# Optimization experiments

Hardware: AMD Instinct MI355X
Metric: run time of the kernel (lower is better)

## Reference

```python
import jax, jax.numpy as jnp
import numpy as np
from jax import lax

EPS = 1e-5
B, T, IN, H, D = 16, 512, 128, 256, 8


def setup_inputs() -> dict:
    key = jax.random.key(0)
    ks = jax.random.split(key, 9)
    s = 0.05  # small init to keep tanh unsaturated
    f32 = jnp.float32
    return {
        "y": jax.random.normal(ks[0], (B, T, IN), f32),
        "W_ih": jax.random.normal(ks[1], (H, IN), f32) * s,
        "W_hh": jax.random.normal(ks[2], (H, H), f32) * s,
        "b_ih": jax.random.normal(ks[3], (H,), f32) * s,
        "b_hh": jax.random.normal(ks[4], (H,), f32) * s,
        "W_mean": jax.random.normal(ks[5], (D, H), f32) * s,
        "b_mean": jax.random.normal(ks[6], (D,), f32) * s,
        "W_bd": jax.random.normal(ks[7], (2 * D, H), f32) * s,
        "b_bd": jax.random.normal(ks[8], (2 * D,), f32) * s,
    }


def _forward(y, W_ih, W_hh, b_ih, b_hh, W_mean, b_mean, W_bd, b_bd):
    # --- single-layer unidirectional tanh RNN (torch nn.RNN, batch_first) ---
    x_proj = jnp.einsum("bti,hi->bth", y, W_ih) + b_ih  # [B,T,H]

    def step(h, xt):
        h_new = jnp.tanh(xt + h @ W_hh.T + b_hh)
        return h_new, h_new

    h0 = jnp.zeros((y.shape[0], W_hh.shape[0]), y.dtype)
    _, hs = lax.scan(step, h0, jnp.swapaxes(x_proj, 0, 1))  # [T,B,H]
    enc = jnp.swapaxes(hs, 0, 1)  # [B,T,H]

    mean = enc @ W_mean.T + b_mean  # [B,T,D]
    bd = enc @ W_bd.T + b_bd        # [B,T,2D]

    d = mean.shape[-1]
    t = bd.shape[1]
    diag_e = bd[:, :, :d]        # [B,T,D]  main-diag factor elems
    off_e = bd[:, :-1, d:]       # [B,T-1,D] super-diag factor elems

    a2 = diag_e ** 2
    b2 = jnp.concatenate([jnp.zeros_like(off_e[:, :1]), off_e ** 2], axis=1)  # [B,T,D]
    ab = diag_e[:, :-1] * off_e  # [B,T-1,D]

    main = jnp.swapaxes(a2 + b2, 1, 2) + EPS  # [B,D,T]  (eps*I folded into diag)
    supd = jnp.swapaxes(ab, 1, 2)             # [B,D,T-1]

    i = jnp.arange(t)
    j = jnp.arange(t - 1)
    prec = jnp.zeros((bd.shape[0], d, t, t), bd.dtype)  # [B,D,T,T]
    prec = prec.at[:, :, i, i].set(main)
    prec = prec.at[:, :, j, j + 1].set(supd)
    prec = prec.at[:, :, j + 1, j].set(supd)
    return mean, prec


def reference(y, W_ih, W_hh, b_ih, b_hh, W_mean, b_mean, W_bd, b_bd):
    # Returns the parameters of the D per-dim MultivariateNormal posteriors:
    # mean [B,T,D] and tridiagonal precision matrices [B,D,T,T].
    return _forward(y, W_ih, W_hh, b_ih, b_hh, W_mean, b_mean, W_bd, b_bd)
```

## Files before the change

kernel.cpp:

```cpp
#include <hip/hip_runtime.h>
#include <math.h>

#define BB 16
#define TT 512
#define IND 128
#define HH 256
#define DD 8
#define EPSF 1e-5f

typedef _Float16 h2_t __attribute__((ext_vector_type(2)));
typedef float f32x4 __attribute__((ext_vector_type(4)));

__device__ __forceinline__ float fast_tanh(float x) {
    const float e = __expf(2.f * x);
    return 1.f - __fdividef(2.f, e + 1.f);
}

__device__ __forceinline__ float dpp_xor1(float x) {
    int i = __builtin_bit_cast(int, x);
    i = __builtin_amdgcn_update_dpp(i, i, 0xB1, 0xF, 0xF, true);
    return __builtin_bit_cast(float, i);
}
__device__ __forceinline__ float dpp_xor2(float x) {
    int i = __builtin_bit_cast(int, x);
    i = __builtin_amdgcn_update_dpp(i, i, 0x4E, 0xF, 0xF, true);
    return __builtin_bit_cast(float, i);
}

__global__ __launch_bounds__(512, 4) void xproj_kernel(
    const float* __restrict__ y, const float* __restrict__ W_ih,
    const float* __restrict__ b_ih, const float* __restrict__ b_hh,
    float* __restrict__ xp)
{
    __shared__ __align__(16) float ylds[16 * IND];
    const int tid = threadIdx.x;
    const int j = tid >> 1;
    const int k4 = (tid & 1) * 4;

    float4 w[16];
    const float* wr = W_ih + (size_t)j * IND + k4;
#pragma unroll
    for (int i = 0; i < 16; ++i) w[i] = *(const float4*)(wr + i * 8);
#pragma unroll
    for (int i = 0; i < 16; ++i)
        asm volatile("" : "+v"(w[i].x), "+v"(w[i].y), "+v"(w[i].z), "+v"(w[i].w));
    const float bias = b_ih[j] + b_hh[j];

    const int row0 = blockIdx.x * 16;
    ((float4*)ylds)[tid] = ((const float4*)(y + (size_t)row0 * IND))[tid];
    __syncthreads();

#pragma unroll 4
    for (int r = 0; r < 16; ++r) {
        const float* yr = ylds + r * IND + k4;
        float a0 = 0.f, a1 = 0.f, a2 = 0.f, a3 = 0.f;
#pragma unroll
        for (int i = 0; i < 16; ++i) {
            const float4 hv = *(const float4*)(yr + i * 8);
            a0 = fmaf(hv.x, w[i].x, a0);
            a1 = fmaf(hv.y, w[i].y, a1);
            a2 = fmaf(hv.z, w[i].z, a2);
            a3 = fmaf(hv.w, w[i].w, a3);
        }
        float acc = (a0 + a1) + (a2 + a3);
        acc += dpp_xor1(acc);
        if ((tid & 1) == 0) xp[(size_t)(row0 + r) * HH + j] = acc + bias;
    }
}

__global__ __launch_bounds__(256, 2) void scan_fill_kernel(
    const float* __restrict__ xp, const float* __restrict__ W_hh,
    float* __restrict__ enc, float* __restrict__ prec)
{
    if (blockIdx.x >= BB) {
        const size_t n4 = (size_t)BB * DD * TT * TT / 4;
        const f32x4 z = {0.f, 0.f, 0.f, 0.f};
        f32x4* p4 = (f32x4*)prec;
        size_t idx = (size_t)(blockIdx.x - BB) * blockDim.x + threadIdx.x;
        const size_t stride = (size_t)(gridDim.x - BB) * blockDim.x;
        for (; idx < n4; idx += stride) p4[idx] = z;
        return;
    }

    const int b   = blockIdx.x;
    const int tid = threadIdx.x;
    const int j0  = tid >> 2;
    const int k   = tid & 3;
    const int jw  = j0 + 64 * k;

    __shared__ __align__(16) char hbufA[4 * 144];
    __shared__ __align__(16) char hbufB[4 * 144];

    h2_t w[4][32];
#pragma unroll
    for (int m = 0; m < 4; ++m) {
        const float* wr = W_hh + (size_t)(j0 + 64 * m) * HH + (size_t)k * 64;
#pragma unroll
        for (int i = 0; i < 32; ++i) {
            h2_t v;
            v.x = (_Float16)wr[2 * i];
            v.y = (_Float16)wr[2 * i + 1];
            w[m][i] = v;
        }
    }
#pragma unroll
    for (int m = 0; m < 4; ++m)
#pragma unroll
        for (int i = 0; i < 32; ++i) {
            int tmp = __builtin_bit_cast(int, w[m][i]);
            asm volatile("" : "+v"(tmp));
            w[m][i] = __builtin_bit_cast(h2_t, tmp);
        }

    if (tid < 128) {
        const int m = 2 * tid;
        h2_t z; z.x = (_Float16)0.f; z.y = (_Float16)0.f;
        *(h2_t*)(hbufA + (m >> 6) * 144 + (m & 63) * 2) = z;
    }

    const float* xpb  = xp  + (size_t)b * TT * HH;

    float xbuf[4];
#pragma unroll
    for (int s = 0; s < 4; ++s) xbuf[s] = xpb[(size_t)s * HH + jw];
    const float* xpf = xpb + (size_t)4 * HH + jw;
    float*      encp = enc + (size_t)b * TT * HH + jw;

    const int roff = k * 144;
    const int hoff = k * 144 + j0 * 2;

    __syncthreads();

    const char* hrd = hbufA;
    char* hwr = hbufB;

#define SCAN_STEP(S, PF)                                                          \
    {                                                                             \
        const float xc = xbuf[S];                                                 \
        if (PF) xbuf[S] = xpf[(S) * HH];                                          \
        float a0 = 0.f, a1 = 0.f, a2 = 0.f, a3 = 0.f;                             \
        const float4* hp = (const float4*)(hrd + roff);                           \
        _Pragma("unroll")                                                         \
        for (int i = 0; i < 8; ++i) {                                             \
            union { float4 f4; h2_t h[4]; } u;                                    \
            u.f4 = hp[i];                                                         \
            _Pragma("unroll")                                                     \
            for (int q = 0; q < 4; ++q) {                                         \
                a0 = __builtin_amdgcn_fdot2(u.h[q], w[0][4 * i + q], a0, false);  \
                a1 = __builtin_amdgcn_fdot2(u.h[q], w[1][4 * i + q], a1, false);  \
                a2 = __builtin_amdgcn_fdot2(u.h[q], w[2][4 * i + q], a2, false);  \
                a3 = __builtin_amdgcn_fdot2(u.h[q], w[3][4 * i + q], a3, false);  \
            }                                                                     \
        }                                                                         \
        a0 += dpp_xor1(a0); a0 += dpp_xor2(a0);                                   \
        a1 += dpp_xor1(a1); a1 += dpp_xor2(a1);                                   \
        a2 += dpp_xor1(a2); a2 += dpp_xor2(a2);                                   \
        a3 += dpp_xor1(a3); a3 += dpp_xor2(a3);                                   \
        const float p = (k & 1) ? ((k & 2) ? a3 : a1) : ((k & 2) ? a2 : a0);      \
        const float hn = fast_tanh(xc + p);                                       \
        encp[(S) * HH] = hn;                                                      \
        *(_Float16*)(hwr + hoff) = (_Float16)hn;                                  \
        asm volatile("s_waitcnt lgkmcnt(0)\n\ts_barrier" ::: "memory");           \
        { const char* tmp_ = hrd; hrd = hwr; hwr = (char*)tmp_; }                 \
    }

    for (int tb = 0; tb < TT - 4; tb += 4) {
        SCAN_STEP(0, 1)
        SCAN_STEP(1, 1)
        SCAN_STEP(2, 1)
        SCAN_STEP(3, 1)
        xpf  += 4 * HH;
        encp += 4 * HH;
    }
    SCAN_STEP(0, 0)
    SCAN_STEP(1, 0)
    SCAN_STEP(2, 0)
    SCAN_STEP(3, 0)
#undef SCAN_STEP
}

__global__ __launch_bounds__(256) void head_kernel(
    const float* __restrict__ enc,
    const float* __restrict__ W_mean, const float* __restrict__ b_mean,
    const float* __restrict__ W_bd, const float* __restrict__ b_bd,
    float* __restrict__ mean_out, float* __restrict__ prec)
{
    const int b = blockIdx.x >> 6;
    const int t0 = (blockIdx.x & 63) * 8;
    __shared__ __align__(16) float erow[9][HH];
    __shared__ float vals[8][32];

    const int tid = threadIdx.x;
    {
        const float4* src = (const float4*)(enc + ((size_t)b * TT + t0) * HH - HH);
        float4* dst = (float4*)erow;
        for (int i = tid; i < 9 * (HH / 4); i += 256) dst[i] = src[i];
    }

    const int g = tid >> 3, m = tid & 7;
    const float* wrow;
    float bias;
    if (g < 8)       { wrow = W_mean + (size_t)g * HH;      bias = b_mean[g]; }
    else if (g < 24) { wrow = W_bd + (size_t)(g - 8) * HH;  bias = b_bd[g - 8]; }
    else             { wrow = W_bd + (size_t)(g - 16) * HH; bias = b_bd[g - 16]; }

    float4 wv[8];
#pragma unroll
    for (int i = 0; i < 8; ++i) wv[i] = ((const float4*)wrow)[m * 8 + i];

    __syncthreads();

    for (int r = 0; r < 8; ++r) {
        const float* src = (g >= 24) ? erow[r] : erow[r + 1];
        float acc = 0.f;
#pragma unroll
        for (int i = 0; i < 8; ++i) {
            const float4 hv = ((const float4*)src)[m * 8 + i];
            acc += wv[i].x * hv.x + wv[i].y * hv.y + wv[i].z * hv.z + wv[i].w * hv.w;
        }
        acc += dpp_xor1(acc);
        acc += dpp_xor2(acc);
        acc += __shfl_xor(acc, 4);
        if (m == 0) vals[r][g] = acc + bias;
    }
    __syncthreads();

    const int r = tid >> 5, s = tid & 31;
    const int t = t0 + r;
    if (s < DD) {
        mean_out[((size_t)b * TT + t) * DD + s] = vals[r][s];
    } else if (s < 2 * DD) {
        const int d = s - DD;
        const float diag = vals[r][8 + d];
        const float off  = vals[r][16 + d];
        const float offp = (t > 0) ? vals[r][24 + d] : 0.f;
        const size_t rowbase = (((size_t)b * DD + d) * TT + t) * TT;
        prec[rowbase + t] = diag * diag + offp * offp + EPSF;
        if (t < TT - 1) {
            const float sv = diag * off;
            prec[rowbase + t + 1] = sv;
            prec[(((size_t)b * DD + d) * TT + (t + 1)) * TT + t] = sv;
        }
    }
}

extern "C" void kernel_launch(void* const* d_in, const int* in_sizes, int n_in,
                              void* d_out, int out_size, void* d_ws, size_t ws_size,
                              hipStream_t stream) {
    const float* y      = (const float*)d_in[0];
    const float* W_ih   = (const float*)d_in[1];
    const float* W_hh   = (const float*)d_in[2];
    const float* b_ih   = (const float*)d_in[3];
    const float* b_hh   = (const float*)d_in[4];
    const float* W_mean = (const float*)d_in[5];
    const float* b_mean = (const float*)d_in[6];
    const float* W_bd   = (const float*)d_in[7];
    const float* b_bd   = (const float*)d_in[8];

    float* out  = (float*)d_out;
    float* mean = out;
    float* prec = out + (size_t)BB * TT * DD;

    float* xp  = (float*)d_ws;
    float* enc = xp + (size_t)BB * TT * HH;

    xproj_kernel<<<512, 512, 0, stream>>>(y, W_ih, b_ih, b_hh, xp);
    scan_fill_kernel<<<1008, 256, 0, stream>>>(xp, W_hh, enc, prec);
    head_kernel<<<1024, 256, 0, stream>>>(enc, W_mean, b_mean, W_bd, b_bd, mean, prec);
}
```

Before: 407.5 us.

## Fuse output heads into RNN scan and skip tridiagonal band in zero fill

Removes the separate head kernel and the enc round-trip through global memory. The scan blocks now compute the mean and bd projections inline each step from the fp16 hidden state in LDS, with a one-step lag so the banded precision entries can be written. The zero-fill blocks skip the tridiagonal band, which avoids write races with the scan-side writes, and the grid shrinks to 512 blocks with launch bounds relaxed to 1. The trade-offs are extra per-step work on the latency-critical serial scan path, extra register pressure, and fp16 precision in the head projections.

```diff
diff --git a/kernel.cpp b/kernel.cpp
--- a/kernel.cpp
+++ b/kernel.cpp
@@ -68,17 +68,32 @@
     }
 }
 
-__global__ __launch_bounds__(256, 2) void scan_fill_kernel(
+__global__ __launch_bounds__(256, 1) void scan_fill_kernel(
     const float* __restrict__ xp, const float* __restrict__ W_hh,
-    float* __restrict__ enc, float* __restrict__ prec)
+    const float* __restrict__ W_mean, const float* __restrict__ b_mean,
+    const float* __restrict__ W_bd, const float* __restrict__ b_bd,
+    float* __restrict__ mean_out, float* __restrict__ prec)
 {
     if (blockIdx.x >= BB) {
-        const size_t n4 = (size_t)BB * DD * TT * TT / 4;
+        const size_t nchunks = (size_t)BB * DD * TT * TT / 4;
         const f32x4 z = {0.f, 0.f, 0.f, 0.f};
-        f32x4* p4 = (f32x4*)prec;
         size_t idx = (size_t)(blockIdx.x - BB) * blockDim.x + threadIdx.x;
         const size_t stride = (size_t)(gridDim.x - BB) * blockDim.x;
-        for (; idx < n4; idx += stride) p4[idx] = z;
+        for (; idx < nchunks; idx += stride) {
+            const int rem = (int)(idx & 65535);
+            const int r  = rem >> 7;
+            const int c0 = (rem & 127) << 2;
+            float* p = prec + idx * 4;
+            if (c0 + 3 < r - 1 || c0 > r + 1) {
+                *(f32x4*)p = z;
+            } else {
+#pragma unroll
+                for (int e = 0; e < 4; ++e) {
+                    const int c = c0 + e;
+                    if (c < r - 1 || c > r + 1) p[e] = 0.f;
+                }
+            }
+        }
         return;
     }
 
@@ -90,6 +105,7 @@
 
     __shared__ __align__(16) char hbufA[4 * 144];
     __shared__ __align__(16) char hbufB[4 * 144];
+    __shared__ float svA[16], svB[16];
 
     h2_t w[4][32];
 #pragma unroll
@@ -112,38 +128,91 @@
             w[m][i] = __builtin_bit_cast(h2_t, tmp);
         }
 
+    const int g    = j0 >> 1;
+    const int sub  = j0 & 1;
+    const bool hv8 = (j0 < 48);
+    const bool headlane = hv8 && ((tid & 7) == 0);
+    const float hbias = hv8 ? ((g < 8) ? b_mean[g] : b_bd[g - 8]) : 0.f;
+
+    h2_t wv[16];
+    {
+        const float* hrow = hv8 ? ((g < 8) ? W_mean + (size_t)g * HH
+                                           : W_bd + (size_t)(g - 8) * HH)
+                                : W_mean;
+        const float* hp0 = hrow + 64 * k + 32 * sub;
+#pragma unroll
+        for (int i = 0; i < 16; ++i) {
+            h2_t v;
+            v.x = (_Float16)hp0[2 * i];
+            v.y = (_Float16)hp0[2 * i + 1];
+            wv[i] = v;
+        }
+    }
+#pragma unroll
+    for (int i = 0; i < 16; ++i) {
+        int tmp = __builtin_bit_cast(int, wv[i]);
+        asm volatile("" : "+v"(tmp));
+        wv[i] = __builtin_bit_cast(h2_t, tmp);
+    }
+
     if (tid < 128) {
         const int m = 2 * tid;
         h2_t z; z.x = (_Float16)0.f; z.y = (_Float16)0.f;
         *(h2_t*)(hbufA + (m >> 6) * 144 + (m & 63) * 2) = z;
     }
 
-    const float* xpb  = xp  + (size_t)b * TT * HH;
-
+    const float* xpb = xp + (size_t)b * TT * HH;
     float xbuf[4];
 #pragma unroll
     for (int s = 0; s < 4; ++s) xbuf[s] = xpb[(size_t)s * HH + jw];
     const float* xpf = xpb + (size_t)4 * HH + jw;
-    float*      encp = enc + (size_t)b * TT * HH + jw;
-
-    const int roff = k * 144;
-    const int hoff = k * 144 + j0 * 2;
+
+    const int roff  = k * 144;
+    const int roff2 = roff + (sub << 6);
+    const int hoff  = k * 144 + j0 * 2;
+
+    float* mpp = mean_out + (size_t)b * TT * DD + (tid >> 3) - DD;
+    float* pr  = prec + ((size_t)b * DD + (tid & 7)) * TT * TT;
+    float offp = 0.f;
 
     __syncthreads();
 
     const char* hrd = hbufA;
     char* hwr = hbufB;
-
-#define SCAN_STEP(S, PF)                                                          \
+    float* svr = svA;
+    float* svw = svB;
+
+#define SCAN_STEP(S, PF, MW, PA)                                                  \
     {                                                                             \
         const float xc = xbuf[S];                                                 \
         if (PF) xbuf[S] = xpf[(S) * HH];                                          \
+        const float4* hp = (const float4*)(hrd + roff);                           \
+        float4 u8[8];                                                             \
+        _Pragma("unroll")                                                         \
+        for (int i = 0; i < 8; ++i) u8[i] = hp[i];                                \
+        float4 uh[4];                                                             \
+        {                                                                         \
+            const float4* hq = (const float4*)(hrd + roff2);                      \
+            _Pragma("unroll")                                                     \
+            for (int i = 0; i < 4; ++i) uh[i] = hq[i];                            \
+        }                                                                         \
+        if (PA) {                                                                 \
+            if (tid < 8) {                                                        \
+                const float dg = svr[tid];                                        \
+                const float of = svr[8 + tid];                                    \
+                pr[0] = dg * dg + offp * offp + EPSF;                             \
+                const float s2 = dg * of;                                         \
+                pr[1] = s2;                                                       \
+                pr[TT] = s2;                                                      \
+                offp = of;                                                        \
+                pr += TT + 1;                                                     \
+            }                                                                     \
+        }                                                                         \
         float a0 = 0.f, a1 = 0.f, a2 = 0.f, a3 = 0.f;                             \
-        const float4* hp = (const float4*)(hrd + roff);                           \
         _Pragma("unroll")                                                         \
         for (int i = 0; i < 8; ++i) {                                             \
             union { float4 f4; h2_t h[4]; } u;                                    \
-            u.f4 = hp[i];                                                         \
+            u.f4 = u8[i];                                                         \
             _Pragma("unroll")                                                     \
             for (int q = 0; q < 4; ++q) {                                         \
                 a0 = __builtin_amdgcn_fdot2(u.h[q], w[0][4 * i + q], a0, false);  \
@@ -152,95 +221,89 @@
                 a3 = __builtin_amdgcn_fdot2(u.h[q], w[3][4 * i + q], a3, false);  \
             }                                                                     \
         }                                                                         \
+        float hacc = 0.f;                                                         \
+        _Pragma("unroll")                                                         \
+        for (int i = 0; i < 4; ++i) {                                             \
+            union { float4 f4; h2_t h[4]; } v;                                    \
+            v.f4 = uh[i];                                                         \
+            _Pragma("unroll")                                                     \
+            for (int q = 0; q < 4; ++q)                                           \
+                hacc = __builtin_amdgcn_fdot2(v.h[q], wv[4 * i + q], hacc, false);\
+        }                                                                         \
         a0 += dpp_xor1(a0); a0 += dpp_xor2(a0);                                   \
         a1 += dpp_xor1(a1); a1 += dpp_xor2(a1);                                   \
         a2 += dpp_xor1(a2); a2 += dpp_xor2(a2);                                   \
         a3 += dpp_xor1(a3); a3 += dpp_xor2(a3);                                   \
+        hacc += dpp_xor1(hacc); hacc += dpp_xor2(hacc);                           \
+        hacc += __shfl_xor(hacc, 4);                                              \
         const float p = (k & 1) ? ((k & 2) ? a3 : a1) : ((k & 2) ? a2 : a0);      \
         const float hn = fast_tanh(xc + p);                                       \
-        encp[(S) * HH] = hn;                                                      \
         *(_Float16*)(hwr + hoff) = (_Float16)hn;                                  \
+        if (headlane) {                                                           \
+            const float S_ = hacc + hbias;                                        \
+            if (g < 8) { if (MW) mpp[0] = S_; }                                   \
+            else svw[g - 8] = S_;                                                 \
+        }                                                                         \
+        mpp += DD;                                                                \
         asm volatile("s_waitcnt lgkmcnt(0)\n\ts_barrier" ::: "memory");           \
-        { const char* tmp_ = hrd; hrd = hwr; hwr = (char*)tmp_; }                 \
-    }
-
-    for (int tb = 0; tb < TT - 4; tb += 4) {
-        SCAN_STEP(0, 1)
-        SCAN_STEP(1, 1)
-        SCAN_STEP(2, 1)
-        SCAN_STEP(3, 1)
-        xpf  += 4 * HH;
-        encp += 4 * HH;
-    }
-    SCAN_STEP(0, 0)
-    SCAN_STEP(1, 0)
-    SCAN_STEP(2, 0)
-    SCAN_STEP(3, 0)
+        { const char* t1 = hrd; hrd = hwr; hwr = (char*)t1; }                     \
+        { float* t2 = svr; svr = svw; svw = t2; }                                 \
+    }
+
+    SCAN_STEP(0, 1, 0, 0)
+    SCAN_STEP(1, 1, 1, 0)
+    SCAN_STEP(2, 1, 1, 1)
+    SCAN_STEP(3, 1, 1, 1)
+    xpf += 4 * HH;
+    for (int tb = 4; tb < TT - 4; tb += 4) {
+        SCAN_STEP(0, 1, 1, 1)
+        SCAN_STEP(1, 1, 1, 1)
+        SCAN_STEP(2, 1, 1, 1)
+        SCAN_STEP(3, 1, 1, 1)
+        xpf += 4 * HH;
+    }
+    SCAN_STEP(0, 0, 1, 1)
+    SCAN_STEP(1, 0, 1, 1)
+    SCAN_STEP(2, 0, 1, 1)
+    SCAN_STEP(3, 0, 1, 1)
 #undef SCAN_STEP
-}
-
-__global__ __launch_bounds__(256) void head_kernel(
-    const float* __restrict__ enc,
-    const float* __restrict__ W_mean, const float* __restrict__ b_mean,
-    const float* __restrict__ W_bd, const float* __restrict__ b_bd,
-    float* __restrict__ mean_out, float* __restrict__ prec)
-{
-    const int b = blockIdx.x >> 6;
-    const int t0 = (blockIdx.x & 63) * 8;
-    __shared__ __align__(16) float erow[9][HH];
-    __shared__ float vals[8][32];
-
-    const int tid = threadIdx.x;
+
+    if (tid < 8) {
+        const float dg = svr[tid];
+        const float of = svr[8 + tid];
+        pr[0] = dg * dg + offp * offp + EPSF;
+        const float s2 = dg * of;
+        pr[1] = s2;
+        pr[TT] = s2;
+        offp = of;
+        pr += TT + 1;
+    }
     {
-        const float4* src = (const float4*)(enc + ((size_t)b * TT + t0) * HH - HH);
-        float4* dst = (float4*)erow;
-        for (int i = tid; i < 9 * (HH / 4); i += 256) dst[i] = src[i];
-    }
-
-    const int g = tid >> 3, m = tid & 7;
-    const float* wrow;
-    float bias;
-    if (g < 8)       { wrow = W_mean + (size_t)g * HH;      bias = b_mean[g]; }
-    else if (g < 24) { wrow = W_bd + (size_t)(g - 8) * HH;  bias = b_bd[g - 8]; }
-    else             { wrow = W_bd + (size_t)(g - 16) * HH; bias = b_bd[g - 16]; }
-
-    float4 wv[8];
-#pragma unroll
-    for (int i = 0; i < 8; ++i) wv[i] = ((const float4*)wrow)[m * 8 + i];
-
-    __syncthreads();
-
-    for (int r = 0; r < 8; ++r) {
-        const float* src = (g >= 24) ? erow[r] : erow[r + 1];
-        float acc = 0.f;
-#pragma unroll
-        for (int i = 0; i < 8; ++i) {
-            const float4 hv = ((const float4*)src)[m * 8 + i];
-            acc += wv[i].x * hv.x + wv[i].y * hv.y + wv[i].z * hv.z + wv[i].w * hv.w;
-        }
-        acc += dpp_xor1(acc);
-        acc += dpp_xor2(acc);
-        acc += __shfl_xor(acc, 4);
-        if (m == 0) vals[r][g] = acc + bias;
-    }
-    __syncthreads();
-
-    const int r = tid >> 5, s = tid & 31;
-    const int t = t0 + r;
-    if (s < DD) {
-        mean_out[((size_t)b * TT + t) * DD + s] = vals[r][s];
-    } else if (s < 2 * DD) {
-        const int d = s - DD;
-        const float diag = vals[r][8 + d];
-        const float off  = vals[r][16 + d];
-        const float offp = (t > 0) ? vals[r][24 + d] : 0.f;
-        const size_t rowbase = (((size_t)b * DD + d) * TT + t) * TT;
-        prec[rowbase + t] = diag * diag + offp * offp + EPSF;
-        if (t < TT - 1) {
-            const float sv = diag * off;
-            prec[rowbase + t + 1] = sv;
-            prec[(((size_t)b * DD + d) * TT + (t + 1)) * TT + t] = sv;
-        }
+        float hacc = 0.f;
+        const float4* hq = (const float4*)(hrd + roff2);
+        float4 uh[4];
+#pragma unroll
+        for (int i = 0; i < 4; ++i) uh[i] = hq[i];
+#pragma unroll
+        for (int i = 0; i < 4; ++i) {
+            union { float4 f4; h2_t h[4]; } v;
+            v.f4 = uh[i];
+#pragma unroll
+            for (int q = 0; q < 4; ++q)
+                hacc = __builtin_amdgcn_fdot2(v.h[q], wv[4 * i + q], hacc, false);
+        }
+        hacc += dpp_xor1(hacc); hacc += dpp_xor2(hacc);
+        hacc += __shfl_xor(hacc, 4);
+        if (headlane) {
+            const float S_ = hacc + hbias;
+            if (g < 8) mpp[0] = S_;
+            else svw[g - 8] = S_;
+        }
+    }
+    asm volatile("s_waitcnt lgkmcnt(0)\n\ts_barrier" ::: "memory");
+    if (tid < 8) {
+        const float dg = svw[tid];
+        pr[0] = dg * dg + offp * offp + EPSF;
     }
 }
 
@@ -261,10 +324,9 @@
     float* mean = out;
     float* prec = out + (size_t)BB * TT * DD;
 
-    float* xp  = (float*)d_ws;
-    float* enc = xp + (size_t)BB * TT * HH;
+    float* xp = (float*)d_ws;
 
     xproj_kernel<<<512, 512, 0, stream>>>(y, W_ih, b_ih, b_hh, xp);
-    scan_fill_kernel<<<1008, 256, 0, stream>>>(xp, W_hh, enc, prec);
-    head_kernel<<<1024, 256, 0, stream>>>(enc, W_mean, b_mean, W_bd, b_bd, mean, prec);
-}
+    scan_fill_kernel<<<512, 256, 0, stream>>>(xp, W_hh, W_mean, b_mean, W_bd, b_bd,
+                                              mean, prec);
+}
```

New measurement: 460.9 us. 1.13x slower.
